# Optimization experiments

Measured on AMD Instinct MI355X. Metric: run time of the kernel, lower is better.

The kernel has to match this reference:

```python
import jax, jax.numpy as jnp
import numpy as np

N, E, F_IN, H, C = 50000, 800000, 128, 4, 32
HC = H * C
NEG_SLOPE = 0.2


def setup_inputs() -> dict:
    key = jax.random.key(0)
    ks = jax.random.split(key, 20)
    def w(k, shape, fan_in):
        return jax.random.normal(k, shape, jnp.float32) * (1.0 / np.sqrt(fan_in))
    inp = {
        'x': jax.random.normal(ks[0], (N, F_IN), jnp.float32),
        'edge_index': jax.random.randint(ks[1], (2, E), 0, N, jnp.int64),
        # layer 1: in F_IN -> H*C
        'Wl1': w(ks[2], (F_IN, HC), F_IN), 'Wr1': w(ks[3], (F_IN, HC), F_IN),
        'att1': w(ks[4], (H, C), C), 'b1': jnp.zeros((HC,), jnp.float32),
        # layer 2: in H*C -> H*C
        'Wl2': w(ks[5], (HC, HC), HC), 'Wr2': w(ks[6], (HC, HC), HC),
        'att2': w(ks[7], (H, C), C), 'b2': jnp.zeros((HC,), jnp.float32),
        # layer 3
        'Wl3': w(ks[8], (HC, HC), HC), 'Wr3': w(ks[9], (HC, HC), HC),
        'att3': w(ks[10], (H, C), C), 'b3': jnp.zeros((HC,), jnp.float32),
        # final fc: H*C -> 1
        'Wf': w(ks[11], (HC, 1), HC), 'bf': jnp.zeros((1,), jnp.float32),
    }
    return inp


def gatv2_layer(x, src, dst, Wl, Wr, att, b):
    n = x.shape[0]
    xl = (x @ Wl).reshape(n, H, C)  # source transform
    xr = (x @ Wr).reshape(n, H, C)  # target transform
    z = xl[src] + xr[dst]                                  # [E', H, C]
    e = jnp.sum(jax.nn.leaky_relu(z, NEG_SLOPE) * att, axis=-1)  # [E', H]
    m = jax.ops.segment_max(e, dst, num_segments=n)        # segment softmax
    a = jnp.exp(e - m[dst])
    denom = jax.ops.segment_sum(a, dst, num_segments=n)
    alpha = a / denom[dst]                                 # [E', H]
    out = jax.ops.segment_sum(alpha[:, :, None] * xl[src], dst, num_segments=n)
    return out.reshape(n, HC) + b


def reference(x, edge_index, Wl1, Wr1, att1, b1, Wl2, Wr2, att2, b2, Wl3, Wr3, att3, b3, Wf, bf):
    n = x.shape[0]
    loops = jnp.arange(n, dtype=edge_index.dtype)
    src = jnp.concatenate([edge_index[0], loops])  # PyG adds self loops
    dst = jnp.concatenate([edge_index[1], loops])
    h = jax.nn.relu(gatv2_layer(x, src, dst, Wl1, Wr1, att1, b1))
    h = jax.nn.relu(gatv2_layer(h, src, dst, Wl2, Wr2, att2, b2))
    h = jax.nn.relu(gatv2_layer(h, src, dst, Wl3, Wr3, att3, b3))
    return (h @ Wf + bf)[:, 0]  # [N]
```

## Files before the change

kernel.cpp:

```cpp
#include <hip/hip_runtime.h>
#include <hip/hip_fp16.h>

constexpr int FDIM = 128;
constexpr float SLOPE = 0.2f;

using half8 = __attribute__((ext_vector_type(8))) _Float16;
using f32x4 = __attribute__((ext_vector_type(4))) float;
using h2v   = __attribute__((ext_vector_type(2))) _Float16;

union H2U { __half2 s; h2v v; unsigned int u; };

__device__ __forceinline__ float fdot2f(h2v a, h2v b, float c) {
  return __builtin_amdgcn_fdot2(a, b, c, false);
}

union U4 { uint4 u; __half2 h[4]; };

__device__ __forceinline__ float edge_logit(const __half2* xa2, const __half2* xr2,
                                            const h2v* att2, h2v c02) {
  float p = 0.f;
#pragma unroll
  for (int j = 0; j < 4; ++j) {
    H2U ua, ur;
    ua.s = xa2[j]; ur.s = xr2[j];
    h2v z = ua.v + ur.v;
    h2v lr = __builtin_elementwise_max(z, z * c02);
    p = fdot2f(lr, att2[j], p);
  }
  return p;
}

__global__ __launch_bounds__(256) void prep_w(
    const float* __restrict__ W0, const float* __restrict__ W1,
    const float* __restrict__ W2, const float* __restrict__ W3,
    const float* __restrict__ W4, const float* __restrict__ W5,
    __half* __restrict__ Wt) {
  const float* Ws[6] = {W0, W1, W2, W3, W4, W5};
  const float* W = Ws[blockIdx.x];
  __half* o = Wt + (size_t)blockIdx.x * FDIM * FDIM;
  const int t = threadIdx.x;
  const int c4 = (t & 31) * 4;
#pragma unroll
  for (int rep = 0; rep < 16; ++rep) {
    int k = (t >> 5) + rep * 8;
    float4 v = *(const float4*)(W + (size_t)k * FDIM + c4);
    o[(size_t)(c4 + 0) * FDIM + k] = __float2half(v.x);
    o[(size_t)(c4 + 1) * FDIM + k] = __float2half(v.y);
    o[(size_t)(c4 + 2) * FDIM + k] = __float2half(v.z);
    o[(size_t)(c4 + 3) * FDIM + k] = __float2half(v.w);
  }
}

template <typename TIN>
__global__ __launch_bounds__(512, 4) void gemm_mfma(
    const TIN* __restrict__ hin, const __half* __restrict__ Wlt,
    const __half* __restrict__ Wrt, __half* __restrict__ xl,
    __half* __restrict__ xr, int n) {
  __shared__ __half Ah[128][40];
  __shared__ __half Bsl[2][128][40];
  const int tid = threadIdx.x;
  const int row0 = blockIdx.x * 128;
  const int wv = tid >> 6;
  const int lane = tid & 63;
  const int sel = wv >> 2;
  const int rb = wv & 3;
  const int l15 = lane & 15;
  const int l4 = lane >> 4;

  f32x4 acc[2][8];
#pragma unroll
  for (int i = 0; i < 2; ++i)
#pragma unroll
    for (int j = 0; j < 8; ++j) acc[i][j] = (f32x4){0.f, 0.f, 0.f, 0.f};

  const int sr = tid >> 2;
  const int sc = (tid & 3) * 8;
  const int bslab = tid >> 8;
  const int bidx = tid & 255;
  const int bc = bidx >> 1;
  const int bko = (bidx & 1) * 16;
  const __half* Wsrc = bslab ? Wrt : Wlt;
  const int gr = row0 + sr;

  for (int k0 = 0; k0 < 128; k0 += 32) {
    if (k0) __syncthreads();
    {
      union { uint4 u; __half h[8]; } pk;
      if constexpr (sizeof(TIN) == 4) {
        float4 v0 = make_float4(0.f, 0.f, 0.f, 0.f), v1 = v0;
        if (gr < n) {
          v0 = *(const float4*)((const float*)hin + (size_t)gr * FDIM + k0 + sc);
          v1 = *(const float4*)((const float*)hin + (size_t)gr * FDIM + k0 + sc + 4);
        }
        pk.h[0] = __float2half(v0.x); pk.h[1] = __float2half(v0.y);
        pk.h[2] = __float2half(v0.z); pk.h[3] = __float2half(v0.w);
        pk.h[4] = __float2half(v1.x); pk.h[5] = __float2half(v1.y);
        pk.h[6] = __float2half(v1.z); pk.h[7] = __float2half(v1.w);
      } else {
        pk.u = make_uint4(0u, 0u, 0u, 0u);
        if (gr < n)
          pk.u = *(const uint4*)((const __half*)hin + (size_t)gr * FDIM + k0 + sc);
      }
      *(uint4*)&Ah[sr][sc] = pk.u;
    }
    {
      const uint4* src = (const uint4*)(Wsrc + (size_t)bc * FDIM + k0 + bko);
      uint4 w0 = src[0], w1 = src[1];
      *(uint4*)&Bsl[bslab][bc][bko] = w0;
      *(uint4*)&Bsl[bslab][bc][bko + 8] = w1;
    }
    __syncthreads();
    half8 a0 = *(const half8*)&Ah[rb * 32 + l15][l4 * 8];
    half8 a1 = *(const half8*)&Ah[rb * 32 + 16 + l15][l4 * 8];
#pragma unroll
    for (int nf = 0; nf < 8; ++nf) {
      half8 b = *(const half8*)&Bsl[sel][nf * 16 + l15][l4 * 8];
      acc[0][nf] = __builtin_amdgcn_mfma_f32_16x16x32_f16(a0, b, acc[0][nf], 0, 0, 0);
      acc[1][nf] = __builtin_amdgcn_mfma_f32_16x16x32_f16(a1, b, acc[1][nf], 0, 0, 0);
    }
  }

  __half* out = sel ? xr : xl;
#pragma unroll
  for (int af = 0; af < 2; ++af) {
#pragma unroll
    for (int nf = 0; nf < 8; ++nf) {
      int col = nf * 16 + l15;
#pragma unroll
      for (int r = 0; r < 4; ++r) {
        int row = row0 + rb * 32 + af * 16 + l4 * 4 + r;
        if (row < n) out[(size_t)row * FDIM + col] = __float2half(acc[af][nf][r]);
      }
    }
  }
}

__global__ __launch_bounds__(256) void hist_dst(const int* __restrict__ dstI,
                                                int* __restrict__ deg, int e_cnt) {
  int i = blockIdx.x * blockDim.x + threadIdx.x;
  int stride = gridDim.x * blockDim.x;
  for (; i < e_cnt; i += stride) atomicAdd(&deg[dstI[i]], 1);
}

__global__ __launch_bounds__(1024) void scan_local(
    const int* __restrict__ deg, int* __restrict__ rowptr,
    int* __restrict__ btot, int n) {
  __shared__ int lds[1024];
  const int t = threadIdx.x;
  const int i = blockIdx.x * 1024 + t;
  int v = (i < n) ? deg[i] : 0;
  lds[t] = v;
  __syncthreads();
  for (int off = 1; off < 1024; off <<= 1) {
    int u = (t >= off) ? lds[t - off] : 0;
    __syncthreads();
    lds[t] += u;
    __syncthreads();
  }
  if (i < n) rowptr[i] = lds[t] - v;
  if (t == 1023) btot[blockIdx.x] = lds[1023];
}

__global__ __launch_bounds__(1024) void scan_btot(int* __restrict__ btot, int nb) {
  __shared__ int lds[1024];
  const int t = threadIdx.x;
  int v = (t < nb) ? btot[t] : 0;
  lds[t] = v;
  __syncthreads();
  for (int off = 1; off < 1024; off <<= 1) {
    int u = (t >= off) ? lds[t - off] : 0;
    __syncthreads();
    lds[t] += u;
    __syncthreads();
  }
  if (t < nb) btot[t] = lds[t] - v;
}

__global__ __launch_bounds__(1024) void scan_add(
    int* __restrict__ rowptr, int* __restrict__ rowcur,
    const int* __restrict__ btot, int n, int e_cnt) {
  const int i = blockIdx.x * 1024 + threadIdx.x;
  if (i < n) {
    int v = rowptr[i] + btot[blockIdx.x];
    rowptr[i] = v;
    rowcur[i] = v;
  }
  if (i == 0) rowptr[n] = e_cnt;
}

__global__ __launch_bounds__(256) void scatter_csr(
    const int* __restrict__ srcI, const int* __restrict__ dstI,
    int* __restrict__ rowcur, int* __restrict__ csr, int e_cnt) {
  int i = blockIdx.x * blockDim.x + threadIdx.x;
  int stride = gridDim.x * blockDim.x;
  for (; i < e_cnt; i += stride) {
    int pos = atomicAdd(&rowcur[dstI[i]], 1);
    csr[pos] = srcI[i];
  }
}

template <int LAST>
__global__ __launch_bounds__(256) void fused_attn(
    const __half* __restrict__ xl, const __half* __restrict__ xr,
    const int* __restrict__ rowptr, const int* __restrict__ csr,
    const float* __restrict__ att, const float* __restrict__ bias,
    const float* __restrict__ Wf, const float* __restrict__ bf,
    void* __restrict__ outp, int n) {
  const int nid = (int)((blockIdx.x * (size_t)blockDim.x + threadIdx.x) >> 6);
  const int lane = threadIdx.x & 63;
  if (nid >= n) return;
  const int g = lane >> 4;
  const int q = lane & 15;
  const int f8 = q * 8;
  const h2v c02 = {(_Float16)SLOPE, (_Float16)SLOPE};
  const float4 aA = *(const float4*)(att + f8);
  const float4 aB = *(const float4*)(att + f8 + 4);
  h2v att2[4] = {{(_Float16)aA.x, (_Float16)aA.y}, {(_Float16)aA.z, (_Float16)aA.w},
                 {(_Float16)aB.x, (_Float16)aB.y}, {(_Float16)aB.z, (_Float16)aB.w}};
  U4 xru, xlu;
  xru.u = *(const uint4*)(xr + (size_t)nid * FDIM + f8);
  xlu.u = *(const uint4*)(xl + (size_t)nid * FDIM + f8);

  float ps = edge_logit(xlu.h, xru.h, att2, c02);
  ps += __shfl_xor(ps, 1);
  ps += __shfl_xor(ps, 2);

  float m = (g == 0) ? ps : -1e30f;
  float s = (g == 0) ? 1.f : 0.f;
  float acc[8];
#pragma unroll
  for (int j = 0; j < 4; ++j) {
    float2 f = __half22float2(xlu.h[j]);
    acc[2 * j] = (g == 0) ? f.x : 0.f;
    acc[2 * j + 1] = (g == 0) ? f.y : 0.f;
  }

  const int rs = rowptr[nid], re = rowptr[nid + 1];
  const int j0 = rs + g;
  bool v0 = j0 < re, v1 = (j0 + 4) < re;
  U4 cur, nx1;
  cur.u = make_uint4(0u, 0u, 0u, 0u);
  nx1.u = cur.u;
  if (v0) cur.u = *(const uint4*)(xl + (size_t)csr[j0] * FDIM + f8);
  if (v1) nx1.u = *(const uint4*)(xl + (size_t)csr[j0 + 4] * FDIM + f8);

  for (int t = rs; t < re; t += 4) {
    const int jn = t + 8 + g;
    const bool vn = jn < re;
    U4 nx2;
    nx2.u = make_uint4(0u, 0u, 0u, 0u);
    if (vn) nx2.u = *(const uint4*)(xl + (size_t)csr[jn] * FDIM + f8);

    float p = edge_logit(cur.h, xru.h, att2, c02);
    p += __shfl_xor(p, 1);
    p += __shfl_xor(p, 2);
    if (v0) {
      float mn = fmaxf(m, p);
      float sc = __expf(m - mn);
      float w = __expf(p - mn);
      s = fmaf(s, sc, w);
#pragma unroll
      for (int j = 0; j < 4; ++j) {
        acc[2 * j] = fmaf(acc[2 * j], sc, w * (float)__low2half(cur.h[j]));
        acc[2 * j + 1] = fmaf(acc[2 * j + 1], sc, w * (float)__high2half(cur.h[j]));
      }
      m = mn;
    }
    v0 = v1; v1 = vn; cur = nx1; nx1 = nx2;
  }

#pragma unroll
  for (int off = 16; off <= 32; off <<= 1) {
    float mo = __shfl_xor(m, off);
    float so = __shfl_xor(s, off);
    float ao[8];
#pragma unroll
    for (int j = 0; j < 8; ++j) ao[j] = __shfl_xor(acc[j], off);
    float M = fmaxf(m, mo);
    float e0 = __expf(m - M), e1 = __expf(mo - M);
    s = fmaf(s, e0, so * e1);
#pragma unroll
    for (int j = 0; j < 8; ++j) acc[j] = fmaf(acc[j], e0, ao[j] * e1);
    m = M;
  }

  const float inv = 1.f / s;
  const float4 bA = *(const float4*)(bias + f8);
  const float4 bB = *(const float4*)(bias + f8 + 4);
  const float bb[8] = {bA.x, bA.y, bA.z, bA.w, bB.x, bB.y, bB.z, bB.w};
  float o[8];
#pragma unroll
  for (int j = 0; j < 8; ++j) o[j] = fmaxf(fmaf(acc[j], inv, bb[j]), 0.f);

  if (LAST == 0) {
    if (g == 0) {
      union { uint4 u; __half2 h[4]; } pk;
#pragma unroll
      for (int j = 0; j < 4; ++j) pk.h[j] = __floats2half2_rn(o[2 * j], o[2 * j + 1]);
      *(uint4*)((__half*)outp + (size_t)nid * FDIM + f8) = pk.u;
    }
  } else {
    const float4 wA = *(const float4*)(Wf + f8);
    const float4 wB = *(const float4*)(Wf + f8 + 4);
    float y = fmaf(o[0], wA.x, fmaf(o[1], wA.y, fmaf(o[2], wA.z,
              fmaf(o[3], wA.w, fmaf(o[4], wB.x, fmaf(o[5], wB.y,
              fmaf(o[6], wB.z, o[7] * wB.w)))))));
    y += __shfl_xor(y, 1);
    y += __shfl_xor(y, 2);
    y += __shfl_xor(y, 4);
    y += __shfl_xor(y, 8);
    if (lane == 0) ((float*)outp)[nid] = y + bf[0];
  }
}

extern "C" void kernel_launch(void* const* d_in, const int* in_sizes, int n_in,
                              void* d_out, int out_size, void* d_ws, size_t ws_size,
                              hipStream_t stream) {
  const float* x = (const float*)d_in[0];
  const int* ei = (const int*)d_in[1];
  const int n = in_sizes[0] / FDIM;
  const int e_cnt = in_sizes[1] / 2;
  const int* srcI = ei;
  const int* dstI = ei + e_cnt;

  const float* Wl[3]  = {(const float*)d_in[2], (const float*)d_in[6], (const float*)d_in[10]};
  const float* Wr[3]  = {(const float*)d_in[3], (const float*)d_in[7], (const float*)d_in[11]};
  const float* att[3] = {(const float*)d_in[4], (const float*)d_in[8], (const float*)d_in[12]};
  const float* bs[3]  = {(const float*)d_in[5], (const float*)d_in[9], (const float*)d_in[13]};
  const float* Wf = (const float*)d_in[14];
  const float* bf = (const float*)d_in[15];

  __half* xlh  = (__half*)d_ws;
  __half* xrh  = xlh + (size_t)n * FDIM;
  __half* hbufh = xrh + (size_t)n * FDIM;
  int* deg    = (int*)(hbufh + (size_t)n * FDIM);
  int* rowptr = deg + n;
  int* rowcur = rowptr + n + 1;
  int* csr    = rowcur + n;
  int* btot   = csr + e_cnt;
  __half* Wt  = (__half*)(btot + 1024);

  const int nb = (n + 1023) / 1024;

  prep_w<<<6, 256, 0, stream>>>(Wl[0], Wr[0], Wl[1], Wr[1], Wl[2], Wr[2], Wt);
  (void)hipMemsetAsync(deg, 0, (size_t)n * sizeof(int), stream);
  hist_dst<<<(e_cnt + 255) / 256, 256, 0, stream>>>(dstI, deg, e_cnt);
  scan_local<<<nb, 1024, 0, stream>>>(deg, rowptr, btot, n);
  scan_btot<<<1, 1024, 0, stream>>>(btot, nb);
  scan_add<<<nb, 1024, 0, stream>>>(rowptr, rowcur, btot, n, e_cnt);
  scatter_csr<<<(e_cnt + 255) / 256, 256, 0, stream>>>(srcI, dstI, rowcur, csr, e_cnt);

  const int gemmGrid = (n + 127) / 128;
  const int nodeBlocks = (n + 3) / 4;

  for (int L = 0; L < 3; ++L) {
    const __half* Wlt = Wt + (size_t)(2 * L) * FDIM * FDIM;
    const __half* Wrt = Wt + (size_t)(2 * L + 1) * FDIM * FDIM;
    if (L == 0)
      gemm_mfma<float><<<gemmGrid, 512, 0, stream>>>(x, Wlt, Wrt, xlh, xrh, n);
    else
      gemm_mfma<__half><<<gemmGrid, 512, 0, stream>>>(hbufh, Wlt, Wrt, xlh, xrh, n);
    if (L < 2) {
      fused_attn<0><<<nodeBlocks, 256, 0, stream>>>(xlh, xrh, rowptr, csr, att[L],
                                                    bs[L], nullptr, nullptr, hbufh, n);
    } else {
      fused_attn<1><<<nodeBlocks, 256, 0, stream>>>(xlh, xrh, rowptr, csr, att[L],
                                                    bs[L], Wf, bf, d_out, n);
    }
  }
}
```

Measured before the change: 379.8 us.

## Load full K into LDS once in GEMM, vectorize stores, deepen gather prefetch

The MFMA projection GEMM now stages the whole 128-wide K dimension of both A and the two weight slabs into LDS in a single pass with one barrier, instead of four 32-wide K steps each with two barriers. The MFMA operands are swapped so each lane's accumulator holds consecutive output columns, which lets the epilogue write 4 halves per 8-byte store instead of scalar half stores. The edge aggregation loop prefetches one more neighbor row, three in flight instead of two, to hide gather latency. The cost is much more LDS per block (about 100 KB) and removal of the occupancy hint, so fewer GEMM blocks fit per CU, plus extra registers in the aggregation kernel.

```diff
diff --git a/kernel.cpp b/kernel.cpp
--- a/kernel.cpp
+++ b/kernel.cpp
@@ -52,12 +52,12 @@
 }
 
 template <typename TIN>
-__global__ __launch_bounds__(512, 4) void gemm_mfma(
+__global__ __launch_bounds__(512) void gemm_mfma(
     const TIN* __restrict__ hin, const __half* __restrict__ Wlt,
     const __half* __restrict__ Wrt, __half* __restrict__ xl,
     __half* __restrict__ xr, int n) {
-  __shared__ __half Ah[128][40];
-  __shared__ __half Bsl[2][128][40];
+  __shared__ __half Ah[128][136];
+  __shared__ __half Bs[2][128][136];
   const int tid = threadIdx.x;
   const int row0 = blockIdx.x * 128;
   const int wv = tid >> 6;
@@ -67,69 +67,77 @@
   const int l15 = lane & 15;
   const int l4 = lane >> 4;
 
-  f32x4 acc[2][8];
-#pragma unroll
-  for (int i = 0; i < 2; ++i)
-#pragma unroll
-    for (int j = 0; j < 8; ++j) acc[i][j] = (f32x4){0.f, 0.f, 0.f, 0.f};
-
-  const int sr = tid >> 2;
-  const int sc = (tid & 3) * 8;
-  const int bslab = tid >> 8;
-  const int bidx = tid & 255;
-  const int bc = bidx >> 1;
-  const int bko = (bidx & 1) * 16;
-  const __half* Wsrc = bslab ? Wrt : Wlt;
-  const int gr = row0 + sr;
-
-  for (int k0 = 0; k0 < 128; k0 += 32) {
-    if (k0) __syncthreads();
-    {
-      union { uint4 u; __half h[8]; } pk;
-      if constexpr (sizeof(TIN) == 4) {
+  {
+    const int r = tid >> 2, q = (tid & 3) * 32;
+    const int gr = row0 + r;
+    if constexpr (sizeof(TIN) == 4) {
+#pragma unroll
+      for (int u = 0; u < 4; ++u) {
         float4 v0 = make_float4(0.f, 0.f, 0.f, 0.f), v1 = v0;
         if (gr < n) {
-          v0 = *(const float4*)((const float*)hin + (size_t)gr * FDIM + k0 + sc);
-          v1 = *(const float4*)((const float*)hin + (size_t)gr * FDIM + k0 + sc + 4);
+          v0 = *(const float4*)((const float*)hin + (size_t)gr * FDIM + q + u * 8);
+          v1 = *(const float4*)((const float*)hin + (size_t)gr * FDIM + q + u * 8 + 4);
         }
+        union { uint4 u4; __half h[8]; } pk;
         pk.h[0] = __float2half(v0.x); pk.h[1] = __float2half(v0.y);
         pk.h[2] = __float2half(v0.z); pk.h[3] = __float2half(v0.w);
         pk.h[4] = __float2half(v1.x); pk.h[5] = __float2half(v1.y);
         pk.h[6] = __float2half(v1.z); pk.h[7] = __float2half(v1.w);
-      } else {
-        pk.u = make_uint4(0u, 0u, 0u, 0u);
+        *(uint4*)&Ah[r][q + u * 8] = pk.u4;
+      }
+    } else {
+#pragma unroll
+      for (int u = 0; u < 4; ++u) {
+        uint4 v = make_uint4(0u, 0u, 0u, 0u);
         if (gr < n)
-          pk.u = *(const uint4*)((const __half*)hin + (size_t)gr * FDIM + k0 + sc);
+          v = *(const uint4*)((const __half*)hin + (size_t)gr * FDIM + q + u * 8);
+        *(uint4*)&Ah[r][q + u * 8] = v;
       }
-      *(uint4*)&Ah[sr][sc] = pk.u;
-    }
-    {
-      const uint4* src = (const uint4*)(Wsrc + (size_t)bc * FDIM + k0 + bko);
-      uint4 w0 = src[0], w1 = src[1];
-      *(uint4*)&Bsl[bslab][bc][bko] = w0;
-      *(uint4*)&Bsl[bslab][bc][bko + 8] = w1;
-    }
-    __syncthreads();
-    half8 a0 = *(const half8*)&Ah[rb * 32 + l15][l4 * 8];
-    half8 a1 = *(const half8*)&Ah[rb * 32 + 16 + l15][l4 * 8];
+    }
+  }
+  {
+    const int slab = tid >> 8;
+    const int idx = tid & 255;
+    const int c = idx >> 1;
+    const int kb = (idx & 1) * 64;
+    const __half* Wsrc = slab ? Wrt : Wlt;
+#pragma unroll
+    for (int u = 0; u < 8; ++u) {
+      uint4 v = *(const uint4*)(Wsrc + (size_t)c * FDIM + kb + u * 8);
+      *(uint4*)&Bs[slab][c][kb + u * 8] = v;
+    }
+  }
+  __syncthreads();
+
+  f32x4 acc[2][8];
+#pragma unroll
+  for (int i = 0; i < 2; ++i)
+#pragma unroll
+    for (int j = 0; j < 8; ++j) acc[i][j] = (f32x4){0.f, 0.f, 0.f, 0.f};
+
+#pragma unroll
+  for (int ks = 0; ks < 4; ++ks) {
+    half8 a0 = *(const half8*)&Ah[rb * 32 + l15][ks * 32 + l4 * 8];
+    half8 a1 = *(const half8*)&Ah[rb * 32 + 16 + l15][ks * 32 + l4 * 8];
 #pragma unroll
     for (int nf = 0; nf < 8; ++nf) {
-      half8 b = *(const half8*)&Bsl[sel][nf * 16 + l15][l4 * 8];
-      acc[0][nf] = __builtin_amdgcn_mfma_f32_16x16x32_f16(a0, b, acc[0][nf], 0, 0, 0);
-      acc[1][nf] = __builtin_amdgcn_mfma_f32_16x16x32_f16(a1, b, acc[1][nf], 0, 0, 0);
+      half8 w = *(const half8*)&Bs[sel][nf * 16 + l15][ks * 32 + l4 * 8];
+      acc[0][nf] = __builtin_amdgcn_mfma_f32_16x16x32_f16(w, a0, acc[0][nf], 0, 0, 0);
+      acc[1][nf] = __builtin_amdgcn_mfma_f32_16x16x32_f16(w, a1, acc[1][nf], 0, 0, 0);
     }
   }
 
   __half* out = sel ? xr : xl;
 #pragma unroll
   for (int af = 0; af < 2; ++af) {
-#pragma unroll
-    for (int nf = 0; nf < 8; ++nf) {
-      int col = nf * 16 + l15;
-#pragma unroll
-      for (int r = 0; r < 4; ++r) {
-        int row = row0 + rb * 32 + af * 16 + l4 * 4 + r;
-        if (row < n) out[(size_t)row * FDIM + col] = __float2half(acc[af][nf][r]);
+    const int row = row0 + rb * 32 + af * 16 + l15;
+    if (row < n) {
+#pragma unroll
+      for (int nf = 0; nf < 8; ++nf) {
+        union { uint2 u; __half2 h[2]; } pk;
+        pk.h[0] = __floats2half2_rn(acc[af][nf][0], acc[af][nf][1]);
+        pk.h[1] = __floats2half2_rn(acc[af][nf][2], acc[af][nf][3]);
+        *(uint2*)(out + (size_t)row * FDIM + nf * 16 + l4 * 4) = pk.u;
       }
     }
   }
@@ -237,19 +245,20 @@
 
   const int rs = rowptr[nid], re = rowptr[nid + 1];
   const int j0 = rs + g;
-  bool v0 = j0 < re, v1 = (j0 + 4) < re;
-  U4 cur, nx1;
+  bool v0 = j0 < re, v1 = (j0 + 4) < re, v2 = (j0 + 8) < re;
+  U4 cur, nx1, nx2;
   cur.u = make_uint4(0u, 0u, 0u, 0u);
-  nx1.u = cur.u;
+  nx1.u = cur.u; nx2.u = cur.u;
   if (v0) cur.u = *(const uint4*)(xl + (size_t)csr[j0] * FDIM + f8);
   if (v1) nx1.u = *(const uint4*)(xl + (size_t)csr[j0 + 4] * FDIM + f8);
+  if (v2) nx2.u = *(const uint4*)(xl + (size_t)csr[j0 + 8] * FDIM + f8);
 
   for (int t = rs; t < re; t += 4) {
-    const int jn = t + 8 + g;
+    const int jn = t + 12 + g;
     const bool vn = jn < re;
-    U4 nx2;
-    nx2.u = make_uint4(0u, 0u, 0u, 0u);
-    if (vn) nx2.u = *(const uint4*)(xl + (size_t)csr[jn] * FDIM + f8);
+    U4 nx3;
+    nx3.u = make_uint4(0u, 0u, 0u, 0u);
+    if (vn) nx3.u = *(const uint4*)(xl + (size_t)csr[jn] * FDIM + f8);
 
     float p = edge_logit(cur.h, xru.h, att2, c02);
     p += __shfl_xor(p, 1);
@@ -266,7 +275,8 @@
       }
       m = mn;
     }
-    v0 = v1; v1 = vn; cur = nx1; nx1 = nx2;
+    v0 = v1; v1 = v2; v2 = vn;
+    cur = nx1; nx1 = nx2; nx2 = nx3;
   }
 
 #pragma unroll
```

After: 404.1 us. +6.4%, slower.
